# Performance work log

Measured on AMD Instinct MI355X. Metric: run time of the kernel, lower is better.

The kernel has to match this reference:

```python
import jax, jax.numpy as jnp
import numpy as np

N_USER = 100000
N_ITEM = 100000
E = 1000000
D_IN = 64
D_OUT = 64


def setup_inputs() -> dict:
    key = jax.random.key(0)
    ks = jax.random.split(key, 10)
    scale = 1.0 / np.sqrt(D_IN)
    return {
        "feat_user": jax.random.normal(ks[0], (N_USER, D_IN), jnp.float32),
        "feat_item": jax.random.normal(ks[1], (N_ITEM, D_IN), jnp.float32),
        "src_clicks": jax.random.randint(ks[2], (E,), 0, N_USER),        # user ids
        "dst_clicks": jax.random.randint(ks[3], (E,), 0, N_ITEM),        # item ids
        "src_clicked_by": jax.random.randint(ks[4], (E,), 0, N_ITEM),    # item ids
        "dst_clicked_by": jax.random.randint(ks[5], (E,), 0, N_USER),    # user ids
        "W_clicks": jax.random.normal(ks[6], (D_OUT, D_IN), jnp.float32) * scale,
        "b_clicks": jax.random.normal(ks[7], (D_OUT,), jnp.float32) * scale,
        "W_clicked_by": jax.random.normal(ks[8], (D_OUT, D_IN), jnp.float32) * scale,
        "b_clicked_by": jax.random.normal(ks[9], (D_OUT,), jnp.float32) * scale,
    }


def _relation_mean(feat_src, W, b, src, dst, n_dst):
    # per-relation Linear on src features (nn.Linear: x @ W.T + b)
    Wh = feat_src @ W.T + b                                  # [N_src, D_OUT]
    # copy_u + mean: gather messages along edges, segment-mean at dst
    msum = jax.ops.segment_sum(Wh[src], dst, num_segments=n_dst)   # [n_dst, D_OUT]
    deg = jax.ops.segment_sum(jnp.ones(src.shape[0], jnp.float32), dst,
                              num_segments=n_dst)                   # [n_dst]
    return msum / jnp.maximum(deg, 1.0)[:, None]             # zero-degree dsts -> 0


def reference(feat_user, feat_item, src_clicks, dst_clicks,
              src_clicked_by, dst_clicked_by,
              W_clicks, b_clicks, W_clicked_by, b_clicked_by):
    # relation (user, clicks, item): messages land on item nodes
    h_item = _relation_mean(feat_user, W_clicks, b_clicks,
                            src_clicks, dst_clicks, N_ITEM)
    # relation (item, clicked_by, user): messages land on user nodes
    h_user = _relation_mean(feat_item, W_clicked_by, b_clicked_by,
                            src_clicked_by, dst_clicked_by, N_USER)
    # cross-relation 'sum' reducer: each ntype receives from exactly one relation here
    return (h_user, h_item)
```

## Files before the change

### kernel.cpp

```cpp
#include <hip/hip_runtime.h>

#define D 64
#define BSH 7
#define BK 128
#define NBK 1024
#define CAP 2048
#define CHUNK 4096
#define EPT (CHUNK / 256)
#define TILE 64

static __device__ __forceinline__ unsigned short f2bf(float x) {
    unsigned int u = __float_as_uint(x);
    unsigned int r = (u + 0x7FFFu + ((u >> 16) & 1u)) >> 16;
    return (unsigned short)r;
}

__global__ __launch_bounds__(256) void phase1(
    const float* __restrict__ feat_u, const float* __restrict__ feat_i,
    const float* __restrict__ W_c, const float* __restrict__ b_c,
    const float* __restrict__ W_cb, const float* __restrict__ b_cb,
    unsigned short* __restrict__ Whb_u, unsigned short* __restrict__ Whb_i,
    const int* __restrict__ srcA, const int* __restrict__ dstA,
    const int* __restrict__ srcB, const int* __restrict__ dstB,
    int* __restrict__ bcur,
    unsigned int* __restrict__ ebufA, unsigned int* __restrict__ ebufB,
    int n_user, int n_item, int n_edges, int ntile, int eb) {
    __shared__ union {
        struct { float FT[TILE * D]; float WT[D * 68]; } lin;
        struct { int hist[NBK], lofs[NBK], lcur[NBK], runb[NBK];
                 unsigned int stage[CHUNK]; unsigned short sbkt[CHUNK];
                 int ps[256]; } fil;
    } sh;
    int t = threadIdx.x;
    int blk = blockIdx.x;

    if (blk < 2 * ntile) {
        int rel = (blk >= ntile);
        int tile = rel ? blk - ntile : blk;
        const float* feat = rel ? feat_i : feat_u;
        const float* W    = rel ? W_cb   : W_c;
        const float* bia  = rel ? b_cb   : b_c;
        unsigned short* out = rel ? Whb_i : Whb_u;
        int n = rel ? n_item : n_user;
        int row0 = tile * TILE;
        if (row0 >= n) return;
        int lr = t >> 4;
        int k4 = (t & 15) * 4;
        #pragma unroll
        for (int it = 0; it < 4; ++it) {
            int r = lr + it * 16;
            int grow = row0 + r; if (grow > n - 1) grow = n - 1;
            float4 f = *(const float4*)(feat + (size_t)grow * D + k4);
            *(float4*)(sh.lin.FT + r * D + k4) = f;
            float4 w = *(const float4*)(W + r * D + k4);
            sh.lin.WT[(k4 + 0) * 68 + r] = w.x;
            sh.lin.WT[(k4 + 1) * 68 + r] = w.y;
            sh.lin.WT[(k4 + 2) * 68 + r] = w.z;
            sh.lin.WT[(k4 + 3) * 68 + r] = w.w;
        }
        __syncthreads();
        int c0 = (t & 15) * 4;
        int r0 = (t >> 4) * 4;
        float4 bv = *(const float4*)(bia + c0);
        float acc[4][4];
        #pragma unroll
        for (int ri = 0; ri < 4; ++ri) {
            acc[ri][0] = bv.x; acc[ri][1] = bv.y; acc[ri][2] = bv.z; acc[ri][3] = bv.w;
        }
        #pragma unroll 4
        for (int k = 0; k < D; ++k) {
            float4 w = *(const float4*)(sh.lin.WT + k * 68 + c0);
            float f0 = sh.lin.FT[(r0 + 0) * D + k];
            float f1 = sh.lin.FT[(r0 + 1) * D + k];
            float f2 = sh.lin.FT[(r0 + 2) * D + k];
            float f3 = sh.lin.FT[(r0 + 3) * D + k];
            acc[0][0] = fmaf(f0, w.x, acc[0][0]); acc[0][1] = fmaf(f0, w.y, acc[0][1]);
            acc[0][2] = fmaf(f0, w.z, acc[0][2]); acc[0][3] = fmaf(f0, w.w, acc[0][3]);
            acc[1][0] = fmaf(f1, w.x, acc[1][0]); acc[1][1] = fmaf(f1, w.y, acc[1][1]);
            acc[1][2] = fmaf(f1, w.z, acc[1][2]); acc[1][3] = fmaf(f1, w.w, acc[1][3]);
            acc[2][0] = fmaf(f2, w.x, acc[2][0]); acc[2][1] = fmaf(f2, w.y, acc[2][1]);
            acc[2][2] = fmaf(f2, w.z, acc[2][2]); acc[2][3] = fmaf(f2, w.w, acc[2][3]);
            acc[3][0] = fmaf(f3, w.x, acc[3][0]); acc[3][1] = fmaf(f3, w.y, acc[3][1]);
            acc[3][2] = fmaf(f3, w.z, acc[3][2]); acc[3][3] = fmaf(f3, w.w, acc[3][3]);
        }
        #pragma unroll
        for (int ri = 0; ri < 4; ++ri) {
            int row = row0 + r0 + ri;
            if (row < n) {
                ushort4 o;
                o.x = f2bf(acc[ri][0]); o.y = f2bf(acc[ri][1]);
                o.z = f2bf(acc[ri][2]); o.w = f2bf(acc[ri][3]);
                *(ushort4*)(out + (size_t)row * D + c0) = o;
            }
        }
    } else {
        int fb = blk - 2 * ntile;
        int rel = (fb >= eb);
        int chunk = rel ? fb - eb : fb;
        const int* src = rel ? srcB : srcA;
        const int* dst = rel ? dstB : dstA;
        int* bu = bcur + rel * NBK;
        unsigned int* ebuf = rel ? ebufB : ebufA;
        for (int i = t; i < NBK; i += 256) sh.fil.hist[i] = 0;
        __syncthreads();
        int base = chunk * CHUNK;
        int m = n_edges - base; if (m > CHUNK) m = CHUNK;
        unsigned int packed[EPT];
        int bk[EPT];
        #pragma unroll
        for (int j = 0; j < EPT; ++j) {
            int e = base + j * 256 + t;
            if (e < n_edges) {
                int d = dst[e];
                int s = src[e];
                bk[j] = ((unsigned)d) >> BSH;
                packed[j] = (unsigned int)s | (((unsigned int)d & (BK - 1)) << 24);
                atomicAdd(&sh.fil.hist[bk[j]], 1);
            } else bk[j] = -1;
        }
        __syncthreads();
        int a[4]; int s4 = 0;
        #pragma unroll
        for (int j = 0; j < 4; ++j) { a[j] = sh.fil.hist[4 * t + j]; s4 += a[j]; }
        sh.fil.ps[t] = s4;
        __syncthreads();
        for (int o = 1; o < 256; o <<= 1) {
            int x = (t >= o) ? sh.fil.ps[t - o] : 0;
            __syncthreads();
            sh.fil.ps[t] += x;
            __syncthreads();
        }
        int ex = sh.fil.ps[t] - s4;
        #pragma unroll
        for (int j = 0; j < 4; ++j) {
            sh.fil.lofs[4 * t + j] = ex; sh.fil.lcur[4 * t + j] = ex;
            ex += a[j];
        }
        __syncthreads();
        for (int b = t; b < NBK; b += 256) {
            int c = sh.fil.hist[b];
            sh.fil.runb[b] = c ? (b * CAP + atomicAdd(&bu[b], c)) : 0;
        }
        #pragma unroll
        for (int j = 0; j < EPT; ++j) {
            if (bk[j] >= 0) {
                int p = atomicAdd(&sh.fil.lcur[bk[j]], 1);
                sh.fil.stage[p] = packed[j];
                sh.fil.sbkt[p] = (unsigned short)bk[j];
            }
        }
        __syncthreads();
        for (int i = t; i < m; i += 256) {
            int b = sh.fil.sbkt[i];
            int pos = sh.fil.runb[b] + (i - sh.fil.lofs[b]);
            if ((unsigned)(pos - b * CAP) < CAP)
                ebuf[pos] = sh.fil.stage[i];
        }
    }
}

__global__ __launch_bounds__(256) void bucket_gather(
    const unsigned short* __restrict__ Whb_u, const unsigned short* __restrict__ Whb_i,
    const unsigned int* __restrict__ ebufA, const unsigned int* __restrict__ ebufB,
    const int* __restrict__ bcur,
    float* __restrict__ h_user, float* __restrict__ h_item,
    int n_user, int n_item) {
    int rel = blockIdx.y;
    const unsigned short* Wh = rel ? Whb_u : Whb_i;
    const unsigned int* ebuf = rel ? ebufB : ebufA;
    float* out = rel ? h_item : h_user;
    int n = rel ? n_item : n_user;
    int b = blockIdx.x;
    int cnt = bcur[rel * NBK + b]; if (cnt > CAP) cnt = CAP;
    size_t base = (size_t)b * CAP;
    __shared__ unsigned int ssrc[CAP];
    __shared__ int hist[BK], ofs[BK], cur[BK];
    int t = threadIdx.x;
    if (t < BK) hist[t] = 0;
    __syncthreads();
    unsigned int pk[CAP / 256];
    #pragma unroll
    for (int j = 0; j < CAP / 256; ++j) {
        int i = t + j * 256;
        if (i < cnt) {
            pk[j] = ebuf[base + i];
            atomicAdd(&hist[pk[j] >> 24], 1);
        }
    }
    __syncthreads();
    if (t < BK) ofs[t] = hist[t];
    __syncthreads();
    for (int o = 1; o < BK; o <<= 1) {
        int x = (t >= o && t < BK) ? ofs[t - o] : 0;
        __syncthreads();
        if (t < BK) ofs[t] += x;
        __syncthreads();
    }
    if (t < BK) { int ex = ofs[t] - hist[t]; ofs[t] = ex; cur[t] = ex; }
    __syncthreads();
    #pragma unroll
    for (int j = 0; j < CAP / 256; ++j) {
        int i = t + j * 256;
        if (i < cnt) {
            int nd = pk[j] >> 24;
            int p = atomicAdd(&cur[nd], 1);
            ssrc[p] = pk[j] & 0xFFFFFFu;
        }
    }
    __syncthreads();
    int lane = t & 63;
    int w = t >> 6;
    int half = lane >> 5;
    int lp = lane & 31;
    int node0 = b * BK;
    for (int nd = w; nd < BK; nd += 4) {
        int node = node0 + nd;
        if (node >= n) break;
        int st = ofs[nd];
        int dg = hist[nd];
        int en = st + dg;
        float l0 = 0.f, l1 = 0.f, l2 = 0.f, l3 = 0.f;
        float h0 = 0.f, h1 = 0.f, h2 = 0.f, h3 = 0.f;
        for (int j = st; j < en; j += 8) {
            int e0 = j + 0 + half, e1 = j + 2 + half, e2 = j + 4 + half, e3 = j + 6 + half;
            unsigned int v0 = 0, v1 = 0, v2 = 0, v3 = 0;
            if (e0 < en) v0 = ((const unsigned int*)(Wh + (size_t)ssrc[e0] * D))[lp];
            if (e1 < en) v1 = ((const unsigned int*)(Wh + (size_t)ssrc[e1] * D))[lp];
            if (e2 < en) v2 = ((const unsigned int*)(Wh + (size_t)ssrc[e2] * D))[lp];
            if (e3 < en) v3 = ((const unsigned int*)(Wh + (size_t)ssrc[e3] * D))[lp];
            l0 += __uint_as_float(v0 << 16); h0 += __uint_as_float(v0 & 0xFFFF0000u);
            l1 += __uint_as_float(v1 << 16); h1 += __uint_as_float(v1 & 0xFFFF0000u);
            l2 += __uint_as_float(v2 << 16); h2 += __uint_as_float(v2 & 0xFFFF0000u);
            l3 += __uint_as_float(v3 << 16); h3 += __uint_as_float(v3 & 0xFFFF0000u);
        }
        float lo = (l0 + l1) + (l2 + l3);
        float hi = (h0 + h1) + (h2 + h3);
        lo += __shfl_xor(lo, 32, 64);
        hi += __shfl_xor(hi, 32, 64);
        if (half == 0) {
            float inv = 1.f / fmaxf((float)dg, 1.f);
            float2 o; o.x = lo * inv; o.y = hi * inv;
            *(float2*)(out + (size_t)node * D + 2 * lp) = o;
        }
    }
}

extern "C" void kernel_launch(void* const* d_in, const int* in_sizes, int n_in,
                              void* d_out, int out_size, void* d_ws, size_t ws_size,
                              hipStream_t stream) {
    const float* feat_user      = (const float*)d_in[0];
    const float* feat_item      = (const float*)d_in[1];
    const int*   src_clicks     = (const int*)d_in[2];
    const int*   dst_clicks     = (const int*)d_in[3];
    const int*   src_clicked_by = (const int*)d_in[4];
    const int*   dst_clicked_by = (const int*)d_in[5];
    const float* W_clicks       = (const float*)d_in[6];
    const float* b_clicks       = (const float*)d_in[7];
    const float* W_clicked_by   = (const float*)d_in[8];
    const float* b_clicked_by   = (const float*)d_in[9];

    const int n_user  = in_sizes[0] / D;
    const int n_item  = in_sizes[1] / D;
    const int n_edges = in_sizes[2];

    float* out = (float*)d_out;
    float* h_user = out;
    float* h_item = out + (size_t)n_user * D;

    unsigned short* Whb_user = (unsigned short*)d_ws;
    unsigned short* Whb_item = Whb_user + (size_t)n_user * D;
    int* ip        = (int*)(Whb_item + (size_t)n_item * D);
    unsigned int* ebuf_user = (unsigned int*)ip;  ip += NBK * CAP;
    unsigned int* ebuf_item = (unsigned int*)ip;  ip += NBK * CAP;
    int* bcur = ip;

    hipMemsetAsync(bcur, 0, 2 * NBK * sizeof(int), stream);

    int ntile = (max(n_user, n_item) + TILE - 1) / TILE;
    int eb = (n_edges + CHUNK - 1) / CHUNK;
    phase1<<<2 * ntile + 2 * eb, 256, 0, stream>>>(
        feat_user, feat_item, W_clicks, b_clicks, W_clicked_by, b_clicked_by,
        Whb_user, Whb_item,
        src_clicked_by, dst_clicked_by, src_clicks, dst_clicks,
        bcur, ebuf_user, ebuf_item,
        n_user, n_item, n_edges, ntile, eb);

    int nbkt = (max(n_user, n_item) + BK - 1) / BK;
    bucket_gather<<<dim3(nbkt, 2), 256, 0, stream>>>(
        Whb_user, Whb_item, ebuf_user, ebuf_item, bcur,
        h_user, h_item, n_user, n_item);
}
```

Before: 230.7 us.

## Halve binning chunk, vectorize edge loads, transpose linear tiles, deepen gather unroll

Several changes land together. The binning chunk shrinks to 2048 edges, which lowers shared memory use and doubles the number of fill blocks. Edge indices are now read as int4 in a per-thread contiguous layout, and the per-bucket output offset is folded into one array. The linear stage stores both the feature and weight tiles transposed so each k-step does two float4 LDS reads, with unroll raised to 8. The gather loop now keeps 8 loads in flight instead of 4, trading extra registers for more memory-level parallelism.

```diff
diff --git a/kernel.cpp b/kernel.cpp
--- a/kernel.cpp
+++ b/kernel.cpp
@@ -5,7 +5,7 @@
 #define BK 128
 #define NBK 1024
 #define CAP 2048
-#define CHUNK 4096
+#define CHUNK 2048
 #define EPT (CHUNK / 256)
 #define TILE 64
 
@@ -26,10 +26,9 @@
     unsigned int* __restrict__ ebufA, unsigned int* __restrict__ ebufB,
     int n_user, int n_item, int n_edges, int ntile, int eb) {
     __shared__ union {
-        struct { float FT[TILE * D]; float WT[D * 68]; } lin;
-        struct { int hist[NBK], lofs[NBK], lcur[NBK], runb[NBK];
-                 unsigned int stage[CHUNK]; unsigned short sbkt[CHUNK];
-                 int ps[256]; } fil;
+        struct { float FT[D * TILE]; float WT[D * TILE]; } lin;
+        struct { int hist[NBK], obase[NBK], cur[NBK], ps[256];
+                 unsigned int stage[CHUNK]; unsigned short sbkt[CHUNK]; } fil;
     } sh;
     int t = threadIdx.x;
     int blk = blockIdx.x;
@@ -51,12 +50,15 @@
             int r = lr + it * 16;
             int grow = row0 + r; if (grow > n - 1) grow = n - 1;
             float4 f = *(const float4*)(feat + (size_t)grow * D + k4);
-            *(float4*)(sh.lin.FT + r * D + k4) = f;
+            sh.lin.FT[(k4 + 0) * TILE + r] = f.x;
+            sh.lin.FT[(k4 + 1) * TILE + r] = f.y;
+            sh.lin.FT[(k4 + 2) * TILE + r] = f.z;
+            sh.lin.FT[(k4 + 3) * TILE + r] = f.w;
             float4 w = *(const float4*)(W + r * D + k4);
-            sh.lin.WT[(k4 + 0) * 68 + r] = w.x;
-            sh.lin.WT[(k4 + 1) * 68 + r] = w.y;
-            sh.lin.WT[(k4 + 2) * 68 + r] = w.z;
-            sh.lin.WT[(k4 + 3) * 68 + r] = w.w;
+            sh.lin.WT[(k4 + 0) * TILE + r] = w.x;
+            sh.lin.WT[(k4 + 1) * TILE + r] = w.y;
+            sh.lin.WT[(k4 + 2) * TILE + r] = w.z;
+            sh.lin.WT[(k4 + 3) * TILE + r] = w.w;
         }
         __syncthreads();
         int c0 = (t & 15) * 4;
@@ -67,21 +69,18 @@
         for (int ri = 0; ri < 4; ++ri) {
             acc[ri][0] = bv.x; acc[ri][1] = bv.y; acc[ri][2] = bv.z; acc[ri][3] = bv.w;
         }
-        #pragma unroll 4
+        #pragma unroll 8
         for (int k = 0; k < D; ++k) {
-            float4 w = *(const float4*)(sh.lin.WT + k * 68 + c0);
-            float f0 = sh.lin.FT[(r0 + 0) * D + k];
-            float f1 = sh.lin.FT[(r0 + 1) * D + k];
-            float f2 = sh.lin.FT[(r0 + 2) * D + k];
-            float f3 = sh.lin.FT[(r0 + 3) * D + k];
-            acc[0][0] = fmaf(f0, w.x, acc[0][0]); acc[0][1] = fmaf(f0, w.y, acc[0][1]);
-            acc[0][2] = fmaf(f0, w.z, acc[0][2]); acc[0][3] = fmaf(f0, w.w, acc[0][3]);
-            acc[1][0] = fmaf(f1, w.x, acc[1][0]); acc[1][1] = fmaf(f1, w.y, acc[1][1]);
-            acc[1][2] = fmaf(f1, w.z, acc[1][2]); acc[1][3] = fmaf(f1, w.w, acc[1][3]);
-            acc[2][0] = fmaf(f2, w.x, acc[2][0]); acc[2][1] = fmaf(f2, w.y, acc[2][1]);
-            acc[2][2] = fmaf(f2, w.z, acc[2][2]); acc[2][3] = fmaf(f2, w.w, acc[2][3]);
-            acc[3][0] = fmaf(f3, w.x, acc[3][0]); acc[3][1] = fmaf(f3, w.y, acc[3][1]);
-            acc[3][2] = fmaf(f3, w.z, acc[3][2]); acc[3][3] = fmaf(f3, w.w, acc[3][3]);
+            float4 w = *(const float4*)(sh.lin.WT + k * TILE + c0);
+            float4 f = *(const float4*)(sh.lin.FT + k * TILE + r0);
+            acc[0][0] = fmaf(f.x, w.x, acc[0][0]); acc[0][1] = fmaf(f.x, w.y, acc[0][1]);
+            acc[0][2] = fmaf(f.x, w.z, acc[0][2]); acc[0][3] = fmaf(f.x, w.w, acc[0][3]);
+            acc[1][0] = fmaf(f.y, w.x, acc[1][0]); acc[1][1] = fmaf(f.y, w.y, acc[1][1]);
+            acc[1][2] = fmaf(f.y, w.z, acc[1][2]); acc[1][3] = fmaf(f.y, w.w, acc[1][3]);
+            acc[2][0] = fmaf(f.z, w.x, acc[2][0]); acc[2][1] = fmaf(f.z, w.y, acc[2][1]);
+            acc[2][2] = fmaf(f.z, w.z, acc[2][2]); acc[2][3] = fmaf(f.z, w.w, acc[2][3]);
+            acc[3][0] = fmaf(f.w, w.x, acc[3][0]); acc[3][1] = fmaf(f.w, w.y, acc[3][1]);
+            acc[3][2] = fmaf(f.w, w.z, acc[3][2]); acc[3][3] = fmaf(f.w, w.w, acc[3][3]);
         }
         #pragma unroll
         for (int ri = 0; ri < 4; ++ri) {
@@ -107,16 +106,35 @@
         int m = n_edges - base; if (m > CHUNK) m = CHUNK;
         unsigned int packed[EPT];
         int bk[EPT];
-        #pragma unroll
-        for (int j = 0; j < EPT; ++j) {
-            int e = base + j * 256 + t;
-            if (e < n_edges) {
-                int d = dst[e];
-                int s = src[e];
-                bk[j] = ((unsigned)d) >> BSH;
-                packed[j] = (unsigned int)s | (((unsigned int)d & (BK - 1)) << 24);
-                atomicAdd(&sh.fil.hist[bk[j]], 1);
-            } else bk[j] = -1;
+        if (m == CHUNK) {
+            const int4* s4p = (const int4*)(src + base);
+            const int4* d4p = (const int4*)(dst + base);
+            #pragma unroll
+            for (int q = 0; q < EPT / 4; ++q) {
+                int4 s = s4p[t * (EPT / 4) + q];
+                int4 dd = d4p[t * (EPT / 4) + q];
+                int sv[4] = {s.x, s.y, s.z, s.w};
+                int dv[4] = {dd.x, dd.y, dd.z, dd.w};
+                #pragma unroll
+                for (int jj = 0; jj < 4; ++jj) {
+                    int j = q * 4 + jj;
+                    bk[j] = ((unsigned)dv[jj]) >> BSH;
+                    packed[j] = (unsigned int)sv[jj] | (((unsigned int)dv[jj] & (BK - 1)) << 24);
+                    atomicAdd(&sh.fil.hist[bk[j]], 1);
+                }
+            }
+        } else {
+            #pragma unroll
+            for (int j = 0; j < EPT; ++j) {
+                int e = base + t * EPT + j;
+                if (e < n_edges) {
+                    int d = dst[e];
+                    int s = src[e];
+                    bk[j] = ((unsigned)d) >> BSH;
+                    packed[j] = (unsigned int)s | (((unsigned int)d & (BK - 1)) << 24);
+                    atomicAdd(&sh.fil.hist[bk[j]], 1);
+                } else bk[j] = -1;
+            }
         }
         __syncthreads();
         int a[4]; int s4 = 0;
@@ -133,18 +151,19 @@
         int ex = sh.fil.ps[t] - s4;
         #pragma unroll
         for (int j = 0; j < 4; ++j) {
-            sh.fil.lofs[4 * t + j] = ex; sh.fil.lcur[4 * t + j] = ex;
+            sh.fil.obase[4 * t + j] = ex;
+            sh.fil.cur[4 * t + j] = ex;
             ex += a[j];
         }
         __syncthreads();
         for (int b = t; b < NBK; b += 256) {
             int c = sh.fil.hist[b];
-            sh.fil.runb[b] = c ? (b * CAP + atomicAdd(&bu[b], c)) : 0;
+            if (c) sh.fil.obase[b] = b * CAP + atomicAdd(&bu[b], c) - sh.fil.obase[b];
         }
         #pragma unroll
         for (int j = 0; j < EPT; ++j) {
             if (bk[j] >= 0) {
-                int p = atomicAdd(&sh.fil.lcur[bk[j]], 1);
+                int p = atomicAdd(&sh.fil.cur[bk[j]], 1);
                 sh.fil.stage[p] = packed[j];
                 sh.fil.sbkt[p] = (unsigned short)bk[j];
             }
@@ -152,7 +171,7 @@
         __syncthreads();
         for (int i = t; i < m; i += 256) {
             int b = sh.fil.sbkt[i];
-            int pos = sh.fil.runb[b] + (i - sh.fil.lofs[b]);
+            int pos = sh.fil.obase[b] + i;
             if ((unsigned)(pos - b * CAP) < CAP)
                 ebuf[pos] = sh.fil.stage[i];
         }
@@ -219,22 +238,25 @@
         int st = ofs[nd];
         int dg = hist[nd];
         int en = st + dg;
-        float l0 = 0.f, l1 = 0.f, l2 = 0.f, l3 = 0.f;
-        float h0 = 0.f, h1 = 0.f, h2 = 0.f, h3 = 0.f;
-        for (int j = st; j < en; j += 8) {
-            int e0 = j + 0 + half, e1 = j + 2 + half, e2 = j + 4 + half, e3 = j + 6 + half;
-            unsigned int v0 = 0, v1 = 0, v2 = 0, v3 = 0;
-            if (e0 < en) v0 = ((const unsigned int*)(Wh + (size_t)ssrc[e0] * D))[lp];
-            if (e1 < en) v1 = ((const unsigned int*)(Wh + (size_t)ssrc[e1] * D))[lp];
-            if (e2 < en) v2 = ((const unsigned int*)(Wh + (size_t)ssrc[e2] * D))[lp];
-            if (e3 < en) v3 = ((const unsigned int*)(Wh + (size_t)ssrc[e3] * D))[lp];
-            l0 += __uint_as_float(v0 << 16); h0 += __uint_as_float(v0 & 0xFFFF0000u);
-            l1 += __uint_as_float(v1 << 16); h1 += __uint_as_float(v1 & 0xFFFF0000u);
-            l2 += __uint_as_float(v2 << 16); h2 += __uint_as_float(v2 & 0xFFFF0000u);
-            l3 += __uint_as_float(v3 << 16); h3 += __uint_as_float(v3 & 0xFFFF0000u);
-        }
-        float lo = (l0 + l1) + (l2 + l3);
-        float hi = (h0 + h1) + (h2 + h3);
+        float l[8], h[8];
+        #pragma unroll
+        for (int q = 0; q < 8; ++q) { l[q] = 0.f; h[q] = 0.f; }
+        for (int j = st; j < en; j += 16) {
+            unsigned int v[8];
+            #pragma unroll
+            for (int q = 0; q < 8; ++q) {
+                int e = j + 2 * q + half;
+                v[q] = 0;
+                if (e < en) v[q] = ((const unsigned int*)(Wh + (size_t)ssrc[e] * D))[lp];
+            }
+            #pragma unroll
+            for (int q = 0; q < 8; ++q) {
+                l[q] += __uint_as_float(v[q] << 16);
+                h[q] += __uint_as_float(v[q] & 0xFFFF0000u);
+            }
+        }
+        float lo = ((l[0] + l[1]) + (l[2] + l[3])) + ((l[4] + l[5]) + (l[6] + l[7]));
+        float hi = ((h[0] + h[1]) + (h[2] + h[3])) + ((h[4] + h[5]) + (h[6] + h[7]));
         lo += __shfl_xor(lo, 32, 64);
         hi += __shfl_xor(hi, 32, 64);
         if (half == 0) {
```

Result: slower. 242.1 us (+4.9%).
